# Kernel tuning notes

Hardware: AMD Instinct MI355X
Metric: run time of the kernel (lower is better)

## Reference

```python
import jax, jax.numpy as jnp
import numpy as np

B, L, D, T, NL = 64, 512, 512, 5000, 2


def setup_inputs() -> dict:
    key = jax.random.key(0)
    k1, k2, k3, k4 = jax.random.split(key, 4)
    enc_output = jax.random.normal(k1, (B, L, D), dtype=jnp.float32)
    # stands in for the row/col-normalized tag co-occurrence matrix (values in [0, 0.01])
    ui_adj = jax.random.uniform(k2, (T, T), dtype=jnp.float32) * 0.01
    # one GCN weight matrix per layer in the layer_stack
    Ws = jax.random.normal(k3, (NL, D, D), dtype=jnp.float32) / np.sqrt(D).astype(np.float32)
    # event ids are 1-indexed in the original (it indexes with e - 1)
    event_type = jax.random.randint(k4, (B, L), 1, T + 1, dtype=jnp.int64)
    slf_attn_mask = jnp.zeros((B, L, L), dtype=bool)
    non_pad_mask = jnp.ones((B, L), dtype=bool)
    return {"enc_output": enc_output, "ui_adj": ui_adj, "Ws": Ws,
            "event_type": event_type, "slf_attn_mask": slf_attn_mask,
            "non_pad_mask": non_pad_mask}


def reference(enc_output, ui_adj, Ws, event_type, slf_attn_mask, non_pad_mask):
    # --- batched per-sample adjacency gather (replaces the Python loop) ---
    idx = event_type - 1                                   # [B, L] 0-indexed
    sub = ui_adj[idx[:, :, None], idx[:, None, :]]         # [B, L, L] = ui_adj[e-1,:][:, e-1]
    diag = ui_adj[idx, idx]                                # [B, L]   = ui_adj[e-1, e-1]
    adj = sub + diag[:, None, :]                           # vector broadcasts across rows, as in torch
    # --- GNN layer stack (hGCN layer ~ relu(A @ X @ W)) ---
    x = enc_output
    for l in range(Ws.shape[0]):                           # small fixed n_layers loop
        x = jax.nn.relu(jnp.einsum('bij,bjd->bid', adj, x) @ Ws[l])
    # --- mean pool over sequence ---
    return x.mean(axis=1)                                  # [B, D]
```

## Files before the change

### kernel.cpp

```cpp
#include <hip/hip_runtime.h>

typedef unsigned short u16;
typedef unsigned int u32;
typedef __bf16 bf16x8 __attribute__((ext_vector_type(8)));
typedef float f32x4 __attribute__((ext_vector_type(4)));
typedef int i32x4 __attribute__((ext_vector_type(4)));

#define T_ 5000
#define CAP 96

__device__ __forceinline__ u16 f2bf(float f) {
  u32 u = __float_as_uint(f);
  u += 0x7fffu + ((u >> 16) & 1u);
  return (u16)(u >> 16);
}
__device__ __forceinline__ float bf2f(u32 bits16) {
  return __uint_as_float(bits16 << 16);
}

__device__ __forceinline__ void gload_lds16(const u16* g, u16* l) {
  __builtin_amdgcn_global_load_lds(
      (__attribute__((address_space(1))) void*)(u16*)g,
      (__attribute__((address_space(3))) void*)l, 16, 0, 0);
}

__device__ __forceinline__ u32 lds_off(const void* p) {
  return (u32)(uintptr_t)(__attribute__((address_space(3))) const void*)p;
}

__global__ void transpose_cast(const float* __restrict__ src, u16* __restrict__ dst) {
  __shared__ float tile[32][33];
  const int tx = threadIdx.x, ty = threadIdx.y;
  const int a0 = blockIdx.x * 32;
  const int b0 = blockIdx.y * 32;
  const size_t zoff = (size_t)blockIdx.z * (512 * 512);
  const float* s = src + zoff;
  u16* d = dst + zoff;
#pragma unroll
  for (int r = 0; r < 4; ++r)
    tile[ty + r * 8][tx] = s[(size_t)(a0 + ty + r * 8) * 512 + b0 + tx];
  __syncthreads();
#pragma unroll
  for (int r = 0; r < 4; ++r)
    d[(size_t)(b0 + ty + r * 8) * 512 + a0 + tx] = f2bf(tile[tx][ty + r * 8]);
}

__global__ void zero_k(int* __restrict__ cnt) {
  const int t = blockIdx.x * 256 + threadIdx.x;
  if (t < 5001) cnt[t] = 0;
}

__global__ void fill_k(const int* __restrict__ ev, const float* __restrict__ ui,
                       int2* __restrict__ cd, int* __restrict__ cnt,
                       int* __restrict__ list, int* __restrict__ ovf) {
  const int t = blockIdx.x * 256 + threadIdx.x;
  const int r = ev[t] - 1;
  int2 v;
  v.x = r;
  v.y = __float_as_int(ui[(size_t)r * (T_ + 1)]);
  cd[t] = v;
  const int pos = atomicAdd(&cnt[r], 1);
  if (pos < CAP) list[r * CAP + pos] = t;
  else { const int o = atomicAdd(&cnt[5000], 1); ovf[o] = t; }
}

__global__ __launch_bounds__(256)
void grow_gather(const float* __restrict__ ui, const int2* __restrict__ cd,
                 const int* __restrict__ cnt, const int* __restrict__ list,
                 u16* __restrict__ adj) {
  const int r = blockIdx.x;
  int c = cnt[r];
  if (c <= 0) return;
  if (c > CAP) c = CAP;
  __shared__ float row[5000];
  const float* __restrict__ src = ui + (size_t)r * T_;
  for (int t = threadIdx.x; t < 1250; t += 256)
    *(float4*)&row[t * 4] = *(const float4*)&src[t * 4];
  __syncthreads();
  const int j = threadIdx.x * 2;
  for (int q = 0; q < c; ++q) {
    const int t = list[r * CAP + q];
    const int base = (t >> 9) << 9;
    const int4 p = *(const int4*)&cd[base + j];
    const float v0 = row[p.x] + __int_as_float(p.y);
    const float v1 = row[p.z] + __int_as_float(p.w);
    const u32 pk = (u32)f2bf(v0) | ((u32)f2bf(v1) << 16);
    *(u32*)&adj[(size_t)t * 512 + j] = pk;
  }
}

__global__ void ovf_gather(const float* __restrict__ ui, const int2* __restrict__ cd,
                           const int* __restrict__ cnt, const int* __restrict__ ovf,
                           u16* __restrict__ adj) {
  const int n = cnt[5000];
  for (int q = blockIdx.x; q < n; q += gridDim.x) {
    const int t = ovf[q];
    const int base = (t >> 9) << 9;
    const long r = (long)cd[t].x;
    const float* __restrict__ row = ui + r * (long)T_;
    const int j = threadIdx.x * 2;
    const int4 p = *(const int4*)&cd[base + j];
    const u32 pk = (u32)f2bf(row[p.x] + __int_as_float(p.y)) |
                   ((u32)f2bf(row[p.z] + __int_as_float(p.w)) << 16);
    *(u32*)&adj[(size_t)t * 512 + j] = pk;
  }
}

template <int MODE>
__global__ __launch_bounds__(512, 2)
void gemm256(const u16* __restrict__ A, const u16* __restrict__ Bm,
             u16* __restrict__ C, size_t strideA, size_t strideB, size_t strideC,
             float* __restrict__ P) {
  extern __shared__ u16 smem[];
  const int tid = threadIdx.x;
  const int lane = tid & 63;
  const int w = tid >> 6;
  const int wm = w >> 2, wn = w & 3;
  const int chunk = gridDim.x >> 3;
  const int wg = blockIdx.x;
  const int mapped = (wg & 7) * chunk + (wg >> 3);
  const int batch = mapped >> 2;
  const int tm = (mapped >> 1) & 1, tn = mapped & 1;
  const int m0 = tm << 8, n0 = tn << 8;
  const u16* __restrict__ Ab = A + (size_t)batch * strideA;
  const u16* __restrict__ Bb = Bm + (size_t)batch * strideB;

  const u16* gA[2];
  const u16* gB[2];
  u32 ldA[2], ldB[2];
#pragma unroll
  for (int r = 0; r < 2; ++r) {
    const int c = r * 512 + tid;
    const int L = c * 16;
    const int p = L >> 7;
    const int off = (L & 127) ^ ((p & 7) << 4);
    const int m = p * 2 + (off >> 6);
    const int kb = off & 63;
    gA[r] = Ab + (size_t)(m0 + m) * 512 + (kb >> 1);
    gB[r] = Bb + (size_t)(n0 + m) * 512 + (kb >> 1);
    ldA[r] = (u32)((r * 512 + w * 64) * 8);
    ldB[r] = (u32)(32768 + (r * 512 + w * 64) * 8);
  }

  const int lr = lane & 15;
  const int kb = (lane >> 4) << 4;
  u32 aOff[8], bOff[4];
#pragma unroll
  for (int m = 0; m < 8; ++m) {
    const int row = wm * 128 + m * 16 + lr;
    aOff[m] = (u32)((row >> 1) * 128 + ((((row & 1) << 6) | kb) ^ (((row >> 1) & 7) << 4)));
  }
#pragma unroll
  for (int n = 0; n < 4; ++n) {
    const int row = wn * 64 + n * 16 + lr;
    bOff[n] = (u32)(65536 + (row >> 1) * 128 + ((((row & 1) << 6) | kb) ^ (((row >> 1) & 7) << 4)));
  }
  const u32 ldsBase = lds_off(smem);

  f32x4 acc[8][4] = {};

  auto stage = [&](int t) {
    const u32 bo = (u32)(t & 3) * 8192;
#pragma unroll
    for (int r = 0; r < 2; ++r) {
      gload_lds16(gA[r] + t * 32, smem + bo + ldA[r]);
      gload_lds16(gB[r] + t * 32, smem + bo + ldB[r]);
    }
  };

  stage(0); stage(1); stage(2);

#pragma unroll
  for (int t = 0; t < 16; ++t) {
    if (t <= 13)      asm volatile("s_waitcnt vmcnt(8)" ::: "memory");
    else if (t == 14) asm volatile("s_waitcnt vmcnt(4)" ::: "memory");
    else              asm volatile("s_waitcnt vmcnt(0)" ::: "memory");
    __builtin_amdgcn_sched_barrier(0);
    if (t + 3 < 16) stage(t + 3);
    asm volatile("" ::: "memory");
    __builtin_amdgcn_s_barrier();
    asm volatile("" ::: "memory");

    const u32 base = ldsBase + (u32)(t & 3) * 16384;
    i32x4 araw[8], braw[4];
#pragma unroll
    for (int m = 0; m < 8; ++m)
      asm volatile("ds_read_b128 %0, %1" : "=v"(araw[m]) : "v"(base + aOff[m]));
#pragma unroll
    for (int n = 0; n < 4; ++n)
      asm volatile("ds_read_b128 %0, %1" : "=v"(braw[n]) : "v"(base + bOff[n]));
    asm volatile("s_waitcnt lgkmcnt(0)" ::: "memory");
    __builtin_amdgcn_sched_barrier(0);

    __builtin_amdgcn_s_setprio(1);
#pragma unroll
    for (int m = 0; m < 8; ++m)
#pragma unroll
      for (int n = 0; n < 4; ++n)
        acc[m][n] = __builtin_amdgcn_mfma_f32_16x16x32_bf16(
            __builtin_bit_cast(bf16x8, araw[m]),
            __builtin_bit_cast(bf16x8, braw[n]), acc[m][n], 0, 0, 0);
    __builtin_amdgcn_s_setprio(0);
    asm volatile("" ::: "memory");
    __builtin_amdgcn_s_barrier();
    __builtin_amdgcn_sched_barrier(0);
  }

  u16* Cb = C + (size_t)batch * strideC;
  if (MODE == 0) {
#pragma unroll
    for (int m = 0; m < 8; ++m) {
      const int row = m0 + wm * 128 + m * 16 + (lane >> 4) * 4;
#pragma unroll
      for (int n = 0; n < 4; ++n) {
        const int col = n0 + wn * 64 + n * 16 + (lane & 15);
        const f32x4 v = acc[m][n];
#pragma unroll
        for (int j = 0; j < 4; ++j)
          Cb[(size_t)(row + j) * 512 + col] = f2bf(v[j]);
      }
    }
  } else if (MODE == 1) {
#pragma unroll
    for (int m = 0; m < 8; ++m) {
      const int i = m0 + wm * 128 + m * 16 + (lane >> 4) * 4;
#pragma unroll
      for (int n = 0; n < 4; ++n) {
        const int d = n0 + wn * 64 + n * 16 + (lane & 15);
        const f32x4 v = acc[m][n];
        uint2 p;
        p.x = (u32)f2bf(fmaxf(v[0], 0.f)) | ((u32)f2bf(fmaxf(v[1], 0.f)) << 16);
        p.y = (u32)f2bf(fmaxf(v[2], 0.f)) | ((u32)f2bf(fmaxf(v[3], 0.f)) << 16);
        *(uint2*)&Cb[(size_t)d * 512 + i] = p;
      }
    }
  } else {
    const int slot = tm * 2 + wm;
#pragma unroll
    for (int n = 0; n < 4; ++n) {
      float s = 0.f;
#pragma unroll
      for (int m = 0; m < 8; ++m) {
        const f32x4 v = acc[m][n];
#pragma unroll
        for (int j = 0; j < 4; ++j) s += fmaxf(v[j], 0.f);
      }
      s += __shfl_xor(s, 16);
      s += __shfl_xor(s, 32);
      if ((lane >> 4) == 0) {
        const int d = n0 + wn * 64 + n * 16 + lane;
        P[((size_t)batch * 4 + slot) * 512 + d] = s;
      }
    }
  }
}

__global__ void reduce_mean(const float* __restrict__ P, float* __restrict__ out) {
  const int t = blockIdx.x * 256 + threadIdx.x;
  const int b = t >> 9, d = t & 511;
  float s = 0.f;
#pragma unroll
  for (int q = 0; q < 4; ++q) s += P[((size_t)b * 4 + q) * 512 + d];
  out[t] = s * (1.0f / 512.0f);
}

extern "C" void kernel_launch(void* const* d_in, const int* in_sizes, int n_in,
                              void* d_out, int out_size, void* d_ws, size_t ws_size,
                              hipStream_t stream) {
  const float* enc = (const float*)d_in[0];
  const float* ui  = (const float*)d_in[1];
  const float* Ws  = (const float*)d_in[2];
  const int*   ev  = (const int*)d_in[3];
  float* out = (float*)d_out;

  char* ws = (char*)d_ws;
  const size_t SLAB = (size_t)64 * 512 * 512 * 2;
  u16* adj  = (u16*)(ws);
  u16* tbuf = (u16*)(ws + SLAB);
  u16* xb   = (u16*)(ws + 2 * SLAB);
  u16* xa   = (u16*)(ws + 3 * SLAB);
  char* p = ws + 4 * SLAB;
  u16* wst  = (u16*)p;  p += (size_t)2 * 512 * 512 * 2;
  int2* cd  = (int2*)p; p += (size_t)32768 * 8;
  int* cnt  = (int*)p;  p += 5008 * 4;
  int* list = (int*)p;  p += (size_t)5000 * CAP * 4;
  int* ovf  = (int*)p;  p += (size_t)32768 * 4;
  float* P  = (float*)p;

  const size_t PS = (size_t)512 * 512;
  const size_t SMEM = 131072;
  (void)hipFuncSetAttribute(reinterpret_cast<const void*>(gemm256<0>),
                            hipFuncAttributeMaxDynamicSharedMemorySize, (int)SMEM);
  (void)hipFuncSetAttribute(reinterpret_cast<const void*>(gemm256<1>),
                            hipFuncAttributeMaxDynamicSharedMemorySize, (int)SMEM);
  (void)hipFuncSetAttribute(reinterpret_cast<const void*>(gemm256<2>),
                            hipFuncAttributeMaxDynamicSharedMemorySize, (int)SMEM);

  zero_k<<<20, 256, 0, stream>>>(cnt);
  fill_k<<<128, 256, 0, stream>>>(ev, ui, cd, cnt, list, ovf);
  transpose_cast<<<dim3(16, 16, 64), dim3(32, 8), 0, stream>>>(enc, xa);
  transpose_cast<<<dim3(16, 16, 2), dim3(32, 8), 0, stream>>>(Ws, wst);
  grow_gather<<<5000, 256, 0, stream>>>(ui, cd, cnt, list, adj);
  ovf_gather<<<8, 256, 0, stream>>>(ui, cd, cnt, ovf, adj);
  gemm256<0><<<256, 512, SMEM, stream>>>(adj, xa, tbuf, PS, PS, PS, nullptr);
  gemm256<1><<<256, 512, SMEM, stream>>>(tbuf, wst, xb, PS, 0, PS, nullptr);
  gemm256<0><<<256, 512, SMEM, stream>>>(adj, xb, tbuf, PS, PS, PS, nullptr);
  gemm256<2><<<256, 512, SMEM, stream>>>(tbuf, wst + PS, nullptr, PS, 0, 0, P);
  reduce_mean<<<128, 256, 0, stream>>>(P, out);
}
```

Measured before the change: 155.7 us.

## Fuse enc_output fp32 transpose-cast into first adjacency GEMM B-operand load

The first batched GEMM now reads enc_output directly as fp32 from global memory into registers, converts it to bf16 with packed-convert instructions, and writes it in transposed, swizzled form into a single LDS B buffer. This removes the separate 64-batch transpose_cast kernel and its bf16 staging slab. The B operand is register-prefetched two stages ahead, with adjusted waitcnt and barrier schedules, while A keeps its async LDS pipeline. The grow_gather loop is also unrolled by two to overlap its gathers, at the cost of more register pressure and extra per-iteration conversion work in the GEMM.

New measurement: 141.1 us, median of 2. 9.4% less time.

```diff
diff --git a/kernel.cpp b/kernel.cpp
--- a/kernel.cpp
+++ b/kernel.cpp
@@ -5,6 +5,8 @@
 typedef __bf16 bf16x8 __attribute__((ext_vector_type(8)));
 typedef float f32x4 __attribute__((ext_vector_type(4)));
 typedef int i32x4 __attribute__((ext_vector_type(4)));
+typedef u32 u32x2 __attribute__((ext_vector_type(2)));
+typedef u32 u32x4 __attribute__((ext_vector_type(4)));
 
 #define T_ 5000
 #define CAP 96
@@ -78,14 +80,27 @@
     *(float4*)&row[t * 4] = *(const float4*)&src[t * 4];
   __syncthreads();
   const int j = threadIdx.x * 2;
-  for (int q = 0; q < c; ++q) {
-    const int t = list[r * CAP + q];
-    const int base = (t >> 9) << 9;
-    const int4 p = *(const int4*)&cd[base + j];
-    const float v0 = row[p.x] + __int_as_float(p.y);
-    const float v1 = row[p.z] + __int_as_float(p.w);
-    const u32 pk = (u32)f2bf(v0) | ((u32)f2bf(v1) << 16);
-    *(u32*)&adj[(size_t)t * 512 + j] = pk;
+  const int lb = r * CAP;
+  int q = 0;
+  for (; q + 2 <= c; q += 2) {
+    const int t0 = list[lb + q], t1 = list[lb + q + 1];
+    const int b0 = (t0 >> 9) << 9, b1 = (t1 >> 9) << 9;
+    const int4 p0 = *(const int4*)&cd[b0 + j];
+    const int4 p1 = *(const int4*)&cd[b1 + j];
+    const u32 pk0 = (u32)f2bf(row[p0.x] + __int_as_float(p0.y)) |
+                    ((u32)f2bf(row[p0.z] + __int_as_float(p0.w)) << 16);
+    const u32 pk1 = (u32)f2bf(row[p1.x] + __int_as_float(p1.y)) |
+                    ((u32)f2bf(row[p1.z] + __int_as_float(p1.w)) << 16);
+    *(u32*)&adj[(size_t)t0 * 512 + j] = pk0;
+    *(u32*)&adj[(size_t)t1 * 512 + j] = pk1;
+  }
+  if (q < c) {
+    const int t0 = list[lb + q];
+    const int b0 = (t0 >> 9) << 9;
+    const int4 p0 = *(const int4*)&cd[b0 + j];
+    const u32 pk0 = (u32)f2bf(row[p0.x] + __int_as_float(p0.y)) |
+                    ((u32)f2bf(row[p0.z] + __int_as_float(p0.w)) << 16);
+    *(u32*)&adj[(size_t)t0 * 512 + j] = pk0;
   }
 }
 
@@ -106,9 +121,9 @@
   }
 }
 
-template <int MODE>
+template <int MODE, int BSRC>
 __global__ __launch_bounds__(512, 2)
-void gemm256(const u16* __restrict__ A, const u16* __restrict__ Bm,
+void gemm256(const u16* __restrict__ A, const void* __restrict__ Bv,
              u16* __restrict__ C, size_t strideA, size_t strideB, size_t strideC,
              float* __restrict__ P) {
   extern __shared__ u16 smem[];
@@ -123,23 +138,73 @@
   const int tm = (mapped >> 1) & 1, tn = mapped & 1;
   const int m0 = tm << 8, n0 = tn << 8;
   const u16* __restrict__ Ab = A + (size_t)batch * strideA;
-  const u16* __restrict__ Bb = Bm + (size_t)batch * strideB;
 
   const u16* gA[2];
-  const u16* gB[2];
-  u32 ldA[2], ldB[2];
+  u32 ldA[2];
 #pragma unroll
   for (int r = 0; r < 2; ++r) {
     const int c = r * 512 + tid;
     const int L = c * 16;
-    const int p = L >> 7;
-    const int off = (L & 127) ^ ((p & 7) << 4);
-    const int m = p * 2 + (off >> 6);
+    const int pp = L >> 7;
+    const int off = (L & 127) ^ ((pp & 7) << 4);
+    const int m = pp * 2 + (off >> 6);
     const int kb = off & 63;
     gA[r] = Ab + (size_t)(m0 + m) * 512 + (kb >> 1);
-    gB[r] = Bb + (size_t)(n0 + m) * 512 + (kb >> 1);
     ldA[r] = (u32)((r * 512 + w * 64) * 8);
-    ldB[r] = (u32)(32768 + (r * 512 + w * 64) * 8);
+  }
+
+  const u16* gB[2] = {nullptr, nullptr};
+  u32 ldB[2] = {0, 0};
+  if (BSRC == 0) {
+    const u16* __restrict__ Bb = (const u16*)Bv + (size_t)batch * strideB;
+#pragma unroll
+    for (int r = 0; r < 2; ++r) {
+      const int c = r * 512 + tid;
+      const int L = c * 16;
+      const int pp = L >> 7;
+      const int off = (L & 127) ^ ((pp & 7) << 4);
+      const int m = pp * 2 + (off >> 6);
+      const int kb = off & 63;
+      gB[r] = Bb + (size_t)(n0 + m) * 512 + (kb >> 1);
+      ldB[r] = (u32)(32768 + (r * 512 + w * 64) * 8);
+    }
+  }
+
+  const int dp = tid & 127;
+  const int lq = tid >> 7;
+  unsigned long long encB = 0;
+  u32 boff0 = 0;
+  u32x2 bs0[8], bs1[8];
+  if (BSRC == 1) {
+    encB = (unsigned long long)(uintptr_t)((const float*)Bv + (size_t)batch * strideB);
+    boff0 = (u32)(((lq * 8) * 512 + n0 + dp * 2) * 4);
+  }
+
+#define BLOAD(t, S)                                                          \
+  {                                                                          \
+    const u32 ob = boff0 + (u32)(t) * 65536u;                                \
+    _Pragma("unroll") for (int i = 0; i < 8; ++i)                            \
+        asm volatile("global_load_dwordx2 %0, %1, %2"                        \
+                     : "=v"(S[i])                                            \
+                     : "v"(ob + (u32)i * 2048u), "s"(encB));                 \
+  }
+
+#define CONVERT_B(S)                                                         \
+  {                                                                          \
+    u32 wrd0[4], wrd1[4];                                                    \
+    _Pragma("unroll") for (int jj = 0; jj < 4; ++jj) {                       \
+      asm("v_cvt_pk_bf16_f32 %0, %1, %2"                                     \
+          : "=v"(wrd0[jj]) : "v"(S[2 * jj].x), "v"(S[2 * jj + 1].x));        \
+      asm("v_cvt_pk_bf16_f32 %0, %1, %2"                                     \
+          : "=v"(wrd1[jj]) : "v"(S[2 * jj].y), "v"(S[2 * jj + 1].y));        \
+    }                                                                        \
+    const u32 by0 = (u32)dp * 128u + ((((u32)lq * 16u)) ^ (((u32)dp & 7u) << 4)); \
+    const u32 by1 = (u32)dp * 128u + ((64u | ((u32)lq * 16u)) ^ (((u32)dp & 7u) << 4)); \
+    u32x4 v0, v1;                                                            \
+    v0.x = wrd0[0]; v0.y = wrd0[1]; v0.z = wrd0[2]; v0.w = wrd0[3];          \
+    v1.x = wrd1[0]; v1.y = wrd1[1]; v1.z = wrd1[2]; v1.w = wrd1[3];          \
+    *(u32x4*)((char*)smem + 65536 + by0) = v0;                               \
+    *(u32x4*)((char*)smem + 65536 + by1) = v1;                               \
   }
 
   const int lr = lane & 15;
@@ -159,36 +224,58 @@
 
   f32x4 acc[8][4] = {};
 
-  auto stage = [&](int t) {
+  auto stageA = [&](int t) {
     const u32 bo = (u32)(t & 3) * 8192;
 #pragma unroll
-    for (int r = 0; r < 2; ++r) {
-      gload_lds16(gA[r] + t * 32, smem + bo + ldA[r]);
-      gload_lds16(gB[r] + t * 32, smem + bo + ldB[r]);
+    for (int r = 0; r < 2; ++r) gload_lds16(gA[r] + t * 32, smem + bo + ldA[r]);
+  };
+  auto stageB0 = [&](int t) {
+    const u32 bo = (u32)(t & 3) * 8192;
+#pragma unroll
+    for (int r = 0; r < 2; ++r) gload_lds16(gB[r] + t * 32, smem + bo + ldB[r]);
+  };
+
+  if (BSRC == 0) {
+    stageA(0); stageB0(0); stageA(1); stageB0(1); stageA(2); stageB0(2);
+  } else {
+    stageA(0); stageA(1); stageA(2);
+    BLOAD(0, bs0); BLOAD(1, bs1);
+  }
+
+#pragma unroll
+  for (int t = 0; t < 16; ++t) {
+    if (BSRC == 0) {
+      if (t <= 13)      asm volatile("s_waitcnt vmcnt(8)" ::: "memory");
+      else if (t == 14) asm volatile("s_waitcnt vmcnt(4)" ::: "memory");
+      else              asm volatile("s_waitcnt vmcnt(0)" ::: "memory");
+      __builtin_amdgcn_sched_barrier(0);
+      if (t + 3 < 16) { stageA(t + 3); stageB0(t + 3); }
+      asm volatile("" ::: "memory");
+      __builtin_amdgcn_s_barrier();
+      asm volatile("" ::: "memory");
+    } else {
+      if (t == 0)              asm volatile("s_waitcnt vmcnt(8)" ::: "memory");
+      else if (t <= 13)        asm volatile("s_waitcnt vmcnt(10)" ::: "memory");
+      else if (t == 14)        asm volatile("s_waitcnt vmcnt(8)" ::: "memory");
+      else                     asm volatile("s_waitcnt vmcnt(0)" ::: "memory");
+      __builtin_amdgcn_sched_barrier(0);
+      if (t & 1) { CONVERT_B(bs1); } else { CONVERT_B(bs0); }
+      if (t + 3 < 16) stageA(t + 3);
+      if (t + 2 < 16) { if (t & 1) { BLOAD(t + 2, bs1); } else { BLOAD(t + 2, bs0); } }
+      asm volatile("s_waitcnt lgkmcnt(0)" ::: "memory");
+      __builtin_amdgcn_s_barrier();
+      asm volatile("" ::: "memory");
     }
-  };
-
-  stage(0); stage(1); stage(2);
-
-#pragma unroll
-  for (int t = 0; t < 16; ++t) {
-    if (t <= 13)      asm volatile("s_waitcnt vmcnt(8)" ::: "memory");
-    else if (t == 14) asm volatile("s_waitcnt vmcnt(4)" ::: "memory");
-    else              asm volatile("s_waitcnt vmcnt(0)" ::: "memory");
-    __builtin_amdgcn_sched_barrier(0);
-    if (t + 3 < 16) stage(t + 3);
-    asm volatile("" ::: "memory");
-    __builtin_amdgcn_s_barrier();
-    asm volatile("" ::: "memory");
-
-    const u32 base = ldsBase + (u32)(t & 3) * 16384;
+
+    const u32 abase = ldsBase + (u32)(t & 3) * 16384;
+    const u32 bbase = (BSRC == 0) ? (ldsBase + (u32)(t & 3) * 16384) : ldsBase;
     i32x4 araw[8], braw[4];
 #pragma unroll
     for (int m = 0; m < 8; ++m)
-      asm volatile("ds_read_b128 %0, %1" : "=v"(araw[m]) : "v"(base + aOff[m]));
+      asm volatile("ds_read_b128 %0, %1" : "=v"(araw[m]) : "v"(abase + aOff[m]));
 #pragma unroll
     for (int n = 0; n < 4; ++n)
-      asm volatile("ds_read_b128 %0, %1" : "=v"(braw[n]) : "v"(base + bOff[n]));
+      asm volatile("ds_read_b128 %0, %1" : "=v"(braw[n]) : "v"(bbase + bOff[n]));
     asm volatile("s_waitcnt lgkmcnt(0)" ::: "memory");
     __builtin_amdgcn_sched_barrier(0);
 
@@ -205,6 +292,8 @@
     __builtin_amdgcn_s_barrier();
     __builtin_amdgcn_sched_barrier(0);
   }
+#undef BLOAD
+#undef CONVERT_B
 
   u16* Cb = C + (size_t)batch * strideC;
   if (MODE == 0) {
@@ -278,8 +367,7 @@
   u16* adj  = (u16*)(ws);
   u16* tbuf = (u16*)(ws + SLAB);
   u16* xb   = (u16*)(ws + 2 * SLAB);
-  u16* xa   = (u16*)(ws + 3 * SLAB);
-  char* p = ws + 4 * SLAB;
+  char* p = ws + 3 * SLAB;
   u16* wst  = (u16*)p;  p += (size_t)2 * 512 * 512 * 2;
   int2* cd  = (int2*)p; p += (size_t)32768 * 8;
   int* cnt  = (int*)p;  p += 5008 * 4;
@@ -288,23 +376,25 @@
   float* P  = (float*)p;
 
   const size_t PS = (size_t)512 * 512;
-  const size_t SMEM = 131072;
-  (void)hipFuncSetAttribute(reinterpret_cast<const void*>(gemm256<0>),
-                            hipFuncAttributeMaxDynamicSharedMemorySize, (int)SMEM);
-  (void)hipFuncSetAttribute(reinterpret_cast<const void*>(gemm256<1>),
-                            hipFuncAttributeMaxDynamicSharedMemorySize, (int)SMEM);
-  (void)hipFuncSetAttribute(reinterpret_cast<const void*>(gemm256<2>),
-                            hipFuncAttributeMaxDynamicSharedMemorySize, (int)SMEM);
+  const size_t SMEM0 = 131072;
+  const size_t SMEM1 = 81920;
+  (void)hipFuncSetAttribute(reinterpret_cast<const void*>(gemm256<0, 1>),
+                            hipFuncAttributeMaxDynamicSharedMemorySize, (int)SMEM1);
+  (void)hipFuncSetAttribute(reinterpret_cast<const void*>(gemm256<1, 0>),
+                            hipFuncAttributeMaxDynamicSharedMemorySize, (int)SMEM0);
+  (void)hipFuncSetAttribute(reinterpret_cast<const void*>(gemm256<0, 0>),
+                            hipFuncAttributeMaxDynamicSharedMemorySize, (int)SMEM0);
+  (void)hipFuncSetAttribute(reinterpret_cast<const void*>(gemm256<2, 0>),
+                            hipFuncAttributeMaxDynamicSharedMemorySize, (int)SMEM0);
 
   zero_k<<<20, 256, 0, stream>>>(cnt);
   fill_k<<<128, 256, 0, stream>>>(ev, ui, cd, cnt, list, ovf);
-  transpose_cast<<<dim3(16, 16, 64), dim3(32, 8), 0, stream>>>(enc, xa);
   transpose_cast<<<dim3(16, 16, 2), dim3(32, 8), 0, stream>>>(Ws, wst);
   grow_gather<<<5000, 256, 0, stream>>>(ui, cd, cnt, list, adj);
   ovf_gather<<<8, 256, 0, stream>>>(ui, cd, cnt, ovf, adj);
-  gemm256<0><<<256, 512, SMEM, stream>>>(adj, xa, tbuf, PS, PS, PS, nullptr);
-  gemm256<1><<<256, 512, SMEM, stream>>>(tbuf, wst, xb, PS, 0, PS, nullptr);
-  gemm256<0><<<256, 512, SMEM, stream>>>(adj, xb, tbuf, PS, PS, PS, nullptr);
-  gemm256<2><<<256, 512, SMEM, stream>>>(tbuf, wst + PS, nullptr, PS, 0, 0, P);
+  gemm256<0, 1><<<256, 512, SMEM1, stream>>>(adj, enc, tbuf, PS, PS, PS, nullptr);
+  gemm256<1, 0><<<256, 512, SMEM0, stream>>>(tbuf, wst, xb, PS, 0, PS, nullptr);
+  gemm256<0, 0><<<256, 512, SMEM0, stream>>>(adj, xb, tbuf, PS, PS, PS, nullptr);
+  gemm256<2, 0><<<256, 512, SMEM0, stream>>>(tbuf, wst + PS, nullptr, PS, 0, 0, P);
   reduce_mean<<<128, 256, 0, stream>>>(P, out);
 }
```
